# Kernel tuning notes

Hardware: AMD Instinct MI355X
Metric: run time of the kernel (lower is better)

## Reference

```python
import jax, jax.numpy as jnp
import numpy as np

D_MODEL = 1024
NUM_HEADS = 16
DEPTH = D_MODEL // NUM_HEADS  # 64
BATCH = 2
SEQ = 2048


def setup_inputs() -> dict:
    key = jax.random.key(0)
    ks = jax.random.split(key, 11)
    s = 0.02
    return {
        "q": jax.random.normal(ks[0], (BATCH, SEQ, D_MODEL), dtype=jnp.float32),
        "k": jax.random.normal(ks[1], (BATCH, SEQ, D_MODEL), dtype=jnp.float32),
        "v": jax.random.normal(ks[2], (BATCH, SEQ, D_MODEL), dtype=jnp.float32),
        "wq": jax.random.normal(ks[3], (D_MODEL, D_MODEL), dtype=jnp.float32) * s,
        "bq": jnp.zeros((D_MODEL,), dtype=jnp.float32),
        "wk": jax.random.normal(ks[4], (D_MODEL, D_MODEL), dtype=jnp.float32) * s,
        "bk": jnp.zeros((D_MODEL,), dtype=jnp.float32),
        "wv": jax.random.normal(ks[5], (D_MODEL, D_MODEL), dtype=jnp.float32) * s,
        "bv": jnp.zeros((D_MODEL,), dtype=jnp.float32),
        "wo": jax.random.normal(ks[6], (D_MODEL, D_MODEL), dtype=jnp.float32) * s,
        "bo": jnp.zeros((D_MODEL,), dtype=jnp.float32),
    }


def reference(q, k, v, wq, bq, wk, bk, wv, bv, wo, bo):
    B = q.shape[0]
    # QKV projections, then split heads: (B, S, H, D)
    qh = (q @ wq + bq).reshape(B, -1, NUM_HEADS, DEPTH)
    kh = (k @ wk + bk).reshape(B, -1, NUM_HEADS, DEPTH)
    vh = (v @ wv + bv).reshape(B, -1, NUM_HEADS, DEPTH)

    inv_sqrt_dk = 1.0 / jnp.sqrt(jnp.float32(DEPTH))
    # scores: (B, Lq, Lk, H)
    scores = jnp.einsum('blhd,bjhd->bljh', qh, kh) * inv_sqrt_dk
    attn = jax.nn.softmax(scores, axis=2)
    # NOTE: original code divides by sqrt(dk) a SECOND time after softmax (faithful quirk)
    attn = attn * inv_sqrt_dk
    out = jnp.einsum('bljh,bjhe->blhe', attn, vh).reshape(B, -1, NUM_HEADS * DEPTH)
    return out @ wo + bo
```

## Files before the change

### kernel.cpp

```cpp
#include <hip/hip_runtime.h>
#include <math.h>

#define D_MODEL 1024
#define NHEADS 16
#define DH 64
#define BATCH 2
#define SEQ 2048
#define M_TOTAL (BATCH * SEQ)

typedef __attribute__((ext_vector_type(8))) short bf16x8;
typedef __attribute__((ext_vector_type(4))) float f32x4;
typedef __attribute__((ext_vector_type(16))) float f32x16;
typedef __attribute__((ext_vector_type(8))) unsigned short ushort8;
typedef unsigned short u16;
typedef unsigned int u32;

#define SCALE_Q 0.18033688f

static __device__ __forceinline__ u16 f2bf(float x) {
  unsigned int u = __float_as_uint(x);
  unsigned int r = (u + 0x7fffu + ((u >> 16) & 1u)) >> 16;
  return (u16)r;
}
static __device__ __forceinline__ u32 pk2bf(float a, float b) {
  return (u32)f2bf(a) | ((u32)f2bf(b) << 16);
}
static __device__ __forceinline__ u32 pkhu(float a, float b) {
  u32 ua = __float_as_uint(a) + 0x8000u;
  u32 ub = __float_as_uint(b) + 0x8000u;
  return (ua >> 16) | (ub & 0xffff0000u);
}
static __device__ __forceinline__ float exp2fast(float x) {
  return __builtin_amdgcn_exp2f(x);
}

static __device__ __forceinline__ void gl_lds16(const u16* g, u16* l) {
  __builtin_amdgcn_global_load_lds(
      (const __attribute__((address_space(1))) u32*)g,
      (__attribute__((address_space(3))) u32*)l, 16, 0, 0);
}

__global__ __launch_bounds__(256) void cvt_kernel(
    const float* __restrict__ q, const float* __restrict__ k, const float* __restrict__ v,
    u16* __restrict__ qb, u16* __restrict__ kb, u16* __restrict__ vb) {
  const int z = blockIdx.z;
  const float* src = (z == 0) ? q : (z == 1) ? k : v;
  u16* dst = (z == 0) ? qb : (z == 1) ? kb : vb;
  const size_t i = ((size_t)blockIdx.x * 256 + threadIdx.x) * 8;
  float4 a = *reinterpret_cast<const float4*>(src + i);
  float4 b = *reinterpret_cast<const float4*>(src + i + 4);
  u32 o0 = pk2bf(a.x, a.y), o1 = pk2bf(a.z, a.w);
  u32 o2 = pk2bf(b.x, b.y), o3 = pk2bf(b.z, b.w);
  *reinterpret_cast<uint4*>(dst + i) = make_uint4(o0, o1, o2, o3);
}

__global__ __launch_bounds__(256) void wtrans_kernel(
    const float* __restrict__ w0, const float* __restrict__ w1,
    const float* __restrict__ w2, const float* __restrict__ w3,
    u16* __restrict__ t0, u16* __restrict__ t1,
    u16* __restrict__ t2, u16* __restrict__ t3) {
  __shared__ float tf[64 * 68];
  const int z = blockIdx.z;
  const float* w = (z == 0) ? w0 : (z == 1) ? w1 : (z == 2) ? w2 : w3;
  u16* wt = (z == 0) ? t0 : (z == 1) ? t1 : (z == 2) ? t2 : t3;
  const int n0 = blockIdx.x * 64, k0 = blockIdx.y * 64;
  const int tid = threadIdx.x;
  const int kl = tid >> 4, nq = (tid & 15) * 4;
#pragma unroll
  for (int c = 0; c < 4; ++c) {
    float4 v = *reinterpret_cast<const float4*>(
        &w[(size_t)(k0 + kl + c * 16) * 1024 + n0 + nq]);
    *reinterpret_cast<float4*>(&tf[(kl + c * 16) * 68 + nq]) = v;
  }
  __syncthreads();
  const int n = tid & 63, kq = tid >> 6;
  u32 pk[8];
#pragma unroll
  for (int p = 0; p < 8; ++p) {
    float a = tf[(kq * 16 + 2 * p) * 68 + n];
    float b = tf[(kq * 16 + 2 * p + 1) * 68 + n];
    pk[p] = pk2bf(a, b);
  }
  u16* dst = &wt[(size_t)(n0 + n) * 1024 + k0 + kq * 16];
  *reinterpret_cast<uint4*>(dst) = make_uint4(pk[0], pk[1], pk[2], pk[3]);
  *reinterpret_cast<uint4*>(dst + 8) = make_uint4(pk[4], pk[5], pk[6], pk[7]);
}

__global__ __launch_bounds__(256) void qkv_gemm_kernel(
    const u16* __restrict__ qb, const u16* __restrict__ kb, const u16* __restrict__ vb,
    const u16* __restrict__ wqT, const u16* __restrict__ wkT, const u16* __restrict__ wvT,
    const float* __restrict__ bq, const float* __restrict__ bk, const float* __restrict__ bv,
    u16* __restrict__ qh, u16* __restrict__ kh, u16* __restrict__ vhT) {
  __shared__ u16 lds[9216];
  u16* sA = lds;
  u16* sB = lds + 4096;

  const int z = blockIdx.z;
  const u16* A  = (z == 0) ? qb : (z == 1) ? kb : vb;
  const u16* BT = (z == 0) ? wqT : (z == 1) ? wkT : wvT;
  const float* bias = (z == 0) ? bq : (z == 1) ? bk : bv;

  int wg = blockIdx.x + 8 * blockIdx.y;
  wg = (wg & 7) * 32 + (wg >> 3);
  const int m0 = (wg >> 3) * 128;
  const int n0 = (wg & 7) * 128;

  const int tid = threadIdx.x;
  const int w = tid >> 6, l = tid & 63;
  const int wr = w >> 1, wc = w & 1;
  const int n = l & 15, g = l >> 4;

  const u16* Ab = A + (size_t)(m0 + w * 16 + (l >> 2)) * 1024 + (l & 3) * 8;
  const u16* Bb = BT + (size_t)(n0 + w * 16 + (l >> 2)) * 1024 + (l & 3) * 8;
  u16* sAb = sA + w * 512;
  u16* sBb = sB + w * 512;

  f32x4 acc[4][4];
#pragma unroll
  for (int fm = 0; fm < 4; ++fm)
#pragma unroll
    for (int fn = 0; fn < 4; ++fn) acc[fm][fn] = (f32x4)(0.0f);

  for (int kk = 0; kk < 1024; kk += 32) {
    __syncthreads();
    gl_lds16(Ab + kk, sAb);
    gl_lds16(Ab + kk + (size_t)64 * 1024, sAb + 2048);
    gl_lds16(Bb + kk, sBb);
    gl_lds16(Bb + kk + (size_t)64 * 1024, sBb + 2048);
    __syncthreads();
    bf16x8 af[4], bf[4];
#pragma unroll
    for (int f = 0; f < 4; ++f)
      af[f] = *reinterpret_cast<const bf16x8*>(&sA[(wr * 64 + f * 16 + n) * 32 + g * 8]);
#pragma unroll
    for (int f = 0; f < 4; ++f)
      bf[f] = *reinterpret_cast<const bf16x8*>(&sB[(wc * 64 + f * 16 + n) * 32 + g * 8]);
#pragma unroll
    for (int fm = 0; fm < 4; ++fm)
#pragma unroll
      for (int fn = 0; fn < 4; ++fn)
        acc[fm][fn] = __builtin_amdgcn_mfma_f32_16x16x32_bf16(af[fm], bf[fn], acc[fm][fn], 0, 0, 0);
  }

  float bv4[4];
#pragma unroll
  for (int fn = 0; fn < 4; ++fn) bv4[fn] = bias[n0 + wc * 64 + fn * 16 + n];

  if (z < 2) {
    const float scale = (z == 0) ? SCALE_Q : 1.0f;
    u16* dst = (z == 0) ? qh : kh;
#pragma unroll
    for (int fm = 0; fm < 4; ++fm)
#pragma unroll
      for (int fn = 0; fn < 4; ++fn)
#pragma unroll
        for (int rr = 0; rr < 4; ++rr) {
          const int row = m0 + wr * 64 + fm * 16 + g * 4 + rr;
          const int col = n0 + wc * 64 + fn * 16 + n;
          dst[(size_t)row * 1024 + col] = f2bf((acc[fm][fn][rr] + bv4[fn]) * scale);
        }
  } else {
    __syncthreads();
    u16* bw = lds + w * 2304;
    const int hh = (n0 >> 6) + wc;
    const int bb = m0 >> 11;
    const int c = l >> 1, half = l & 1;
    const int sbase = (m0 & 2047) + wr * 64 + half * 32;
#pragma unroll
    for (int p = 0; p < 2; ++p) {
#pragma unroll
      for (int fh = 0; fh < 2; ++fh) {
        const int fn = p * 2 + fh;
#pragma unroll
        for (int fm = 0; fm < 4; ++fm)
#pragma unroll
          for (int rr = 0; rr < 4; ++rr)
            bw[(fh * 16 + n) * 72 + fm * 16 + g * 4 + rr] =
                f2bf(acc[fm][fn][rr] + bv4[fn]);
      }
      __syncthreads();
      u16* gd = vhT + ((size_t)((bb * NHEADS + hh) * DH + p * 32 + c)) * SEQ + sbase;
#pragma unroll
      for (int j = 0; j < 4; ++j)
        *reinterpret_cast<uint4*>(gd + j * 8) =
            *reinterpret_cast<const uint4*>(&bw[c * 72 + half * 32 + j * 8]);
      __syncthreads();
    }
  }
}

__global__ __launch_bounds__(256) void out_gemm_kernel(
    const u16* __restrict__ aob, const u16* __restrict__ woT,
    const float* __restrict__ bo, float* __restrict__ out) {
  __shared__ u16 lds[6144];
  u16* sA = lds;
  u16* sB = lds + 4096;

  int wg = blockIdx.x + 16 * blockIdx.y;
  wg = (wg & 7) * 64 + (wg >> 3);
  const int m0 = (wg >> 4) * 128;
  const int n0 = (wg & 15) * 64;

  const int tid = threadIdx.x;
  const int w = tid >> 6, l = tid & 63;
  const int wr = w >> 1, wc = w & 1;
  const int n = l & 15, g = l >> 4;

  const u16* Ab = aob + (size_t)(m0 + w * 16 + (l >> 2)) * 1024 + (l & 3) * 8;
  const u16* Bb = woT + (size_t)(n0 + w * 16 + (l >> 2)) * 1024 + (l & 3) * 8;
  u16* sAb = sA + w * 512;
  u16* sBb = sB + w * 512;

  f32x4 acc[4][2];
#pragma unroll
  for (int fm = 0; fm < 4; ++fm)
#pragma unroll
    for (int fn = 0; fn < 2; ++fn) acc[fm][fn] = (f32x4)(0.0f);

  for (int kk = 0; kk < 1024; kk += 32) {
    __syncthreads();
    gl_lds16(Ab + kk, sAb);
    gl_lds16(Ab + kk + (size_t)64 * 1024, sAb + 2048);
    gl_lds16(Bb + kk, sBb);
    __syncthreads();
    bf16x8 af[4], bf[2];
#pragma unroll
    for (int f = 0; f < 4; ++f)
      af[f] = *reinterpret_cast<const bf16x8*>(&sA[(wr * 64 + f * 16 + n) * 32 + g * 8]);
#pragma unroll
    for (int f = 0; f < 2; ++f)
      bf[f] = *reinterpret_cast<const bf16x8*>(&sB[(wc * 32 + f * 16 + n) * 32 + g * 8]);
#pragma unroll
    for (int fm = 0; fm < 4; ++fm)
#pragma unroll
      for (int fn = 0; fn < 2; ++fn)
        acc[fm][fn] = __builtin_amdgcn_mfma_f32_16x16x32_bf16(af[fm], bf[fn], acc[fm][fn], 0, 0, 0);
  }

  const float b0 = bo[n0 + wc * 32 + n];
  const float b1 = bo[n0 + wc * 32 + 16 + n];
#pragma unroll
  for (int fm = 0; fm < 4; ++fm)
#pragma unroll
    for (int rr = 0; rr < 4; ++rr) {
      const int row = m0 + wr * 64 + fm * 16 + g * 4 + rr;
      out[(size_t)row * 1024 + n0 + wc * 32 + n] = acc[fm][0][rr] + b0;
      out[(size_t)row * 1024 + n0 + wc * 32 + 16 + n] = acc[fm][1][rr] + b1;
    }
}

#define KT 64
__global__ __launch_bounds__(256, 2) void attn_mfma_kernel(
    const u16* __restrict__ qh, const u16* __restrict__ kh,
    const u16* __restrict__ vhT, u16* __restrict__ aob) {
  const int bid = blockIdx.x;
  const int xcd = bid & 7;
  const int idx = bid >> 3;
  const int bh = (xcd << 2) | (idx >> 4);
  const int qt = idx & 15;
  const int b = bh >> 4, h = bh & 15;

  const int tid = threadIdx.x;
  const int w = tid >> 6, l = tid & 63;
  const int lr = l & 31;
  const int g1 = l >> 5;
  const int q0 = qt * 128 + w * 32;

  __shared__ u16 Ks[2][KT * DH];
  __shared__ u16 Vs[2][DH * KT];
  __shared__ float Ls[4][32];

  bf16x8 qf[4];
#pragma unroll
  for (int kq = 0; kq < 4; ++kq)
    qf[kq] = *reinterpret_cast<const bf16x8*>(
        &qh[((size_t)(b * SEQ + q0 + lr)) * D_MODEL + h * DH + kq * 16 + g1 * 8]);

  f32x16 O0 = (f32x16)(0.0f), O1 = (f32x16)(0.0f);
  float lsum = 0.0f;

  const int srow = tid >> 2, sq = tid & 3;
  const u16* kp0 = kh + (size_t)(b * SEQ + srow) * D_MODEL + h * DH + sq * 16;
  const u16* vp0 = vhT + ((size_t)((b * NHEADS + h) * DH + srow)) * SEQ + sq * 16;
  const int sbase = srow * 64 + sq * 16;
  const int sxor = (srow & 7) << 3;
  const int rxor = (lr & 7) << 3;

  ushort8 kr[2], vr[2];
#pragma unroll
  for (int c = 0; c < 2; ++c) {
    kr[c] = *reinterpret_cast<const ushort8*>(kp0 + c * 8);
    vr[c] = *reinterpret_cast<const ushort8*>(vp0 + c * 8);
  }
#pragma unroll
  for (int c = 0; c < 2; ++c) {
    const int sidx = (sbase + c * 8) ^ sxor;
    *reinterpret_cast<ushort8*>(&Ks[0][sidx]) = kr[c];
    *reinterpret_cast<ushort8*>(&Vs[0][sidx]) = vr[c];
  }
  __syncthreads();

  int cur = 0;
  for (int jt = 0; jt < SEQ / KT; ++jt) {
    if (jt + 1 < SEQ / KT) {
      const int off = (jt + 1) * KT;
#pragma unroll
      for (int c = 0; c < 2; ++c) {
        kr[c] = *reinterpret_cast<const ushort8*>(kp0 + (size_t)off * D_MODEL + c * 8);
        vr[c] = *reinterpret_cast<const ushort8*>(vp0 + off + c * 8);
      }
    }

    __builtin_amdgcn_s_setprio(1);
    f32x16 St0 = (f32x16)(0.0f), St1 = (f32x16)(0.0f);
#pragma unroll
    for (int kq = 0; kq < 4; ++kq) {
      const int coff = kq * 16 + g1 * 8;
      bf16x8 kf0 = *reinterpret_cast<const bf16x8*>(&Ks[cur][(lr * 64 + coff) ^ rxor]);
      bf16x8 kf1 = *reinterpret_cast<const bf16x8*>(&Ks[cur][((32 + lr) * 64 + coff) ^ rxor]);
      St0 = __builtin_amdgcn_mfma_f32_32x32x16_bf16(kf0, qf[kq], St0, 0, 0, 0);
      St1 = __builtin_amdgcn_mfma_f32_32x32x16_bf16(kf1, qf[kq], St1, 0, 0, 0);
    }
    __builtin_amdgcn_s_setprio(0);

    u32 U0[8], U1[8];
#pragma unroll
    for (int s = 0; s < 8; ++s) {
      float a0 = exp2fast(St0[2 * s]), b0 = exp2fast(St0[2 * s + 1]);
      float a1 = exp2fast(St1[2 * s]), b1 = exp2fast(St1[2 * s + 1]);
      lsum += (a0 + b0) + (a1 + b1);
      U0[s] = pkhu(a0, b0);
      U1[s] = pkhu(a1, b1);
    }

    __builtin_amdgcn_s_setprio(1);
#pragma unroll
    for (int kb2 = 0; kb2 < 2; ++kb2) {
#pragma unroll
      for (int m16 = 0; m16 < 2; ++m16) {
        union { u32 u[4]; bf16x8 v; } pa;
        if (kb2 == 0) {
          pa.u[0] = U0[m16 * 4 + 0]; pa.u[1] = U0[m16 * 4 + 1];
          pa.u[2] = U0[m16 * 4 + 2]; pa.u[3] = U0[m16 * 4 + 3];
        } else {
          pa.u[0] = U1[m16 * 4 + 0]; pa.u[1] = U1[m16 * 4 + 1];
          pa.u[2] = U1[m16 * 4 + 2]; pa.u[3] = U1[m16 * 4 + 3];
        }
        const int koff = kb2 * 32 + m16 * 16 + g1 * 4;
        union { u32 u[4]; bf16x8 v; } vb0, vb1;
        *reinterpret_cast<uint2*>(&vb0.u[0]) =
            *reinterpret_cast<const uint2*>(&Vs[cur][(lr * 64 + koff) ^ rxor]);
        *reinterpret_cast<uint2*>(&vb0.u[2]) =
            *reinterpret_cast<const uint2*>(&Vs[cur][(lr * 64 + koff + 8) ^ rxor]);
        *reinterpret_cast<uint2*>(&vb1.u[0]) =
            *reinterpret_cast<const uint2*>(&Vs[cur][((32 + lr) * 64 + koff) ^ rxor]);
        *reinterpret_cast<uint2*>(&vb1.u[2]) =
            *reinterpret_cast<const uint2*>(&Vs[cur][((32 + lr) * 64 + koff + 8) ^ rxor]);
        O0 = __builtin_amdgcn_mfma_f32_32x32x16_bf16(pa.v, vb0.v, O0, 0, 0, 0);
        O1 = __builtin_amdgcn_mfma_f32_32x32x16_bf16(pa.v, vb1.v, O1, 0, 0, 0);
      }
    }
    __builtin_amdgcn_s_setprio(0);

    if (jt + 1 < SEQ / KT) {
#pragma unroll
      for (int c = 0; c < 2; ++c) {
        const int sidx = (sbase + c * 8) ^ sxor;
        *reinterpret_cast<ushort8*>(&Ks[cur ^ 1][sidx]) = kr[c];
        *reinterpret_cast<ushort8*>(&Vs[cur ^ 1][sidx]) = vr[c];
      }
    }
    __syncthreads();
    cur ^= 1;
  }

  lsum += (float)__shfl_xor(lsum, 32);
  if (g1 == 0) Ls[w][lr] = lsum;
  float invr[16];
#pragma unroll
  for (int c = 0; c < 4; ++c) {
    float4 lv = *reinterpret_cast<const float4*>(&Ls[w][c * 8 + g1 * 4]);
    invr[c * 4 + 0] = 0.125f / lv.x;
    invr[c * 4 + 1] = 0.125f / lv.y;
    invr[c * 4 + 2] = 0.125f / lv.z;
    invr[c * 4 + 3] = 0.125f / lv.w;
  }
#pragma unroll
  for (int dblk = 0; dblk < 2; ++dblk) {
#pragma unroll
    for (int s = 0; s < 8; ++s) {
      const int r0 = 2 * s, r1 = 2 * s + 1;
      float x0 = (dblk ? O1[r0] : O0[r0]) * invr[r0];
      float x1 = (dblk ? O1[r1] : O0[r1]) * invr[r1];
      const int row0 = q0 + (r0 & 3) + 8 * (r0 >> 2) + 4 * g1;
      const int row1 = q0 + (r1 & 3) + 8 * (r1 >> 2) + 4 * g1;
      const int col = h * DH + dblk * 32 + lr;
      aob[((size_t)(b * SEQ + row0)) * D_MODEL + col] = f2bf(x0);
      aob[((size_t)(b * SEQ + row1)) * D_MODEL + col] = f2bf(x1);
    }
  }
}

extern "C" void kernel_launch(void* const* d_in, const int* in_sizes, int n_in,
                              void* d_out, int out_size, void* d_ws, size_t ws_size,
                              hipStream_t stream) {
  const float* q  = (const float*)d_in[0];
  const float* k  = (const float*)d_in[1];
  const float* v  = (const float*)d_in[2];
  const float* wq = (const float*)d_in[3];
  const float* bq = (const float*)d_in[4];
  const float* wk = (const float*)d_in[5];
  const float* bk = (const float*)d_in[6];
  const float* wv = (const float*)d_in[7];
  const float* bv = (const float*)d_in[8];
  const float* wo = (const float*)d_in[9];
  const float* bo = (const float*)d_in[10];
  float* out = (float*)d_out;

  const size_t wcount = (size_t)D_MODEL * D_MODEL;
  const size_t tcount = (size_t)M_TOTAL * D_MODEL;
  u16* wqT = (u16*)d_ws;
  u16* wkT = wqT + wcount;
  u16* wvT = wkT + wcount;
  u16* woT = wvT + wcount;
  u16* qb  = woT + wcount;
  u16* kb  = qb + tcount;
  u16* vb  = kb + tcount;
  u16* qh  = vb + tcount;
  u16* kh  = qh + tcount;
  u16* vhT = kh + tcount;
  u16* aob = qb;

  dim3 blk(256);

  cvt_kernel<<<dim3(2048, 1, 3), blk, 0, stream>>>(q, k, v, qb, kb, vb);
  wtrans_kernel<<<dim3(16, 16, 4), blk, 0, stream>>>(wq, wk, wv, wo, wqT, wkT, wvT, woT);

  qkv_gemm_kernel<<<dim3(8, 32, 3), blk, 0, stream>>>(
      qb, kb, vb, wqT, wkT, wvT, bq, bk, bv, qh, kh, vhT);

  attn_mfma_kernel<<<dim3(512), dim3(256), 0, stream>>>(qh, kh, vhT, aob);

  out_gemm_kernel<<<dim3(16, 32), blk, 0, stream>>>(aob, woT, bo, out);
}
```

Measured before the change: 136.7 us.

## Merge prep kernels, compute softmax row sums via MFMA, use perm packing

Fuses the fp32-to-bf16 activation conversion and weight transpose into one launch, saving a kernel launch and its tail. In attention, the softmax denominator is now accumulated by an extra MFMA of the bf16 probabilities against a ones vector. This replaces the per-element VALU adds, the cross-lane shuffle and the LDS exchange. The bf16 packing uses a single v_perm. The trade-off is one extra MFMA per PV step and row sums built from rounded bf16 probabilities. The prep grid also launches many idle blocks for the weight slices.

```diff
diff --git a/kernel.cpp b/kernel.cpp
--- a/kernel.cpp
+++ b/kernel.cpp
@@ -26,9 +26,8 @@
   return (u32)f2bf(a) | ((u32)f2bf(b) << 16);
 }
 static __device__ __forceinline__ u32 pkhu(float a, float b) {
-  u32 ua = __float_as_uint(a) + 0x8000u;
-  u32 ub = __float_as_uint(b) + 0x8000u;
-  return (ua >> 16) | (ub & 0xffff0000u);
+  return __builtin_amdgcn_perm(__float_as_uint(b) + 0x8000u,
+                               __float_as_uint(a) + 0x8000u, 0x07060302u);
 }
 static __device__ __forceinline__ float exp2fast(float x) {
   return __builtin_amdgcn_exp2f(x);
@@ -40,37 +39,38 @@
       (__attribute__((address_space(3))) u32*)l, 16, 0, 0);
 }
 
-__global__ __launch_bounds__(256) void cvt_kernel(
+__global__ __launch_bounds__(256) void prep_kernel(
     const float* __restrict__ q, const float* __restrict__ k, const float* __restrict__ v,
-    u16* __restrict__ qb, u16* __restrict__ kb, u16* __restrict__ vb) {
-  const int z = blockIdx.z;
-  const float* src = (z == 0) ? q : (z == 1) ? k : v;
-  u16* dst = (z == 0) ? qb : (z == 1) ? kb : vb;
-  const size_t i = ((size_t)blockIdx.x * 256 + threadIdx.x) * 8;
-  float4 a = *reinterpret_cast<const float4*>(src + i);
-  float4 b = *reinterpret_cast<const float4*>(src + i + 4);
-  u32 o0 = pk2bf(a.x, a.y), o1 = pk2bf(a.z, a.w);
-  u32 o2 = pk2bf(b.x, b.y), o3 = pk2bf(b.z, b.w);
-  *reinterpret_cast<uint4*>(dst + i) = make_uint4(o0, o1, o2, o3);
-}
-
-__global__ __launch_bounds__(256) void wtrans_kernel(
+    u16* __restrict__ qb, u16* __restrict__ kb, u16* __restrict__ vb,
     const float* __restrict__ w0, const float* __restrict__ w1,
     const float* __restrict__ w2, const float* __restrict__ w3,
     u16* __restrict__ t0, u16* __restrict__ t1,
     u16* __restrict__ t2, u16* __restrict__ t3) {
   __shared__ float tf[64 * 68];
   const int z = blockIdx.z;
-  const float* w = (z == 0) ? w0 : (z == 1) ? w1 : (z == 2) ? w2 : w3;
-  u16* wt = (z == 0) ? t0 : (z == 1) ? t1 : (z == 2) ? t2 : t3;
-  const int n0 = blockIdx.x * 64, k0 = blockIdx.y * 64;
   const int tid = threadIdx.x;
+  if (z < 3) {
+    const float* src = (z == 0) ? q : (z == 1) ? k : v;
+    u16* dst = (z == 0) ? qb : (z == 1) ? kb : vb;
+    const size_t i = ((size_t)blockIdx.x * 256 + tid) * 8;
+    float4 a = *reinterpret_cast<const float4*>(src + i);
+    float4 b = *reinterpret_cast<const float4*>(src + i + 4);
+    u32 o0 = pk2bf(a.x, a.y), o1 = pk2bf(a.z, a.w);
+    u32 o2 = pk2bf(b.x, b.y), o3 = pk2bf(b.z, b.w);
+    *reinterpret_cast<uint4*>(dst + i) = make_uint4(o0, o1, o2, o3);
+    return;
+  }
+  if (blockIdx.x >= 256) return;
+  const int zz = z - 3;
+  const float* w = (zz == 0) ? w0 : (zz == 1) ? w1 : (zz == 2) ? w2 : w3;
+  u16* wt = (zz == 0) ? t0 : (zz == 1) ? t1 : (zz == 2) ? t2 : t3;
+  const int n0 = (blockIdx.x & 15) * 64, k0 = (blockIdx.x >> 4) * 64;
   const int kl = tid >> 4, nq = (tid & 15) * 4;
 #pragma unroll
   for (int c = 0; c < 4; ++c) {
-    float4 v = *reinterpret_cast<const float4*>(
+    float4 vv = *reinterpret_cast<const float4*>(
         &w[(size_t)(k0 + kl + c * 16) * 1024 + n0 + nq]);
-    *reinterpret_cast<float4*>(&tf[(kl + c * 16) * 68 + nq]) = v;
+    *reinterpret_cast<float4*>(&tf[(kl + c * 16) * 68 + nq]) = vv;
   }
   __syncthreads();
   const int n = tid & 63, kq = tid >> 6;
@@ -268,7 +268,9 @@
 
   __shared__ u16 Ks[2][KT * DH];
   __shared__ u16 Vs[2][DH * KT];
-  __shared__ float Ls[4][32];
+
+  union { u32 u[4]; bf16x8 v; } onesu;
+  onesu.u[0] = onesu.u[1] = onesu.u[2] = onesu.u[3] = 0x3F803F80u;
 
   bf16x8 qf[4];
 #pragma unroll
@@ -276,8 +278,7 @@
     qf[kq] = *reinterpret_cast<const bf16x8*>(
         &qh[((size_t)(b * SEQ + q0 + lr)) * D_MODEL + h * DH + kq * 16 + g1 * 8]);
 
-  f32x16 O0 = (f32x16)(0.0f), O1 = (f32x16)(0.0f);
-  float lsum = 0.0f;
+  f32x16 O0 = (f32x16)(0.0f), O1 = (f32x16)(0.0f), L0 = (f32x16)(0.0f);
 
   const int srow = tid >> 2, sq = tid & 3;
   const u16* kp0 = kh + (size_t)(b * SEQ + srow) * D_MODEL + h * DH + sq * 16;
@@ -328,7 +329,6 @@
     for (int s = 0; s < 8; ++s) {
       float a0 = exp2fast(St0[2 * s]), b0 = exp2fast(St0[2 * s + 1]);
       float a1 = exp2fast(St1[2 * s]), b1 = exp2fast(St1[2 * s + 1]);
-      lsum += (a0 + b0) + (a1 + b1);
       U0[s] = pkhu(a0, b0);
       U1[s] = pkhu(a1, b1);
     }
@@ -358,6 +358,7 @@
             *reinterpret_cast<const uint2*>(&Vs[cur][((32 + lr) * 64 + koff + 8) ^ rxor]);
         O0 = __builtin_amdgcn_mfma_f32_32x32x16_bf16(pa.v, vb0.v, O0, 0, 0, 0);
         O1 = __builtin_amdgcn_mfma_f32_32x32x16_bf16(pa.v, vb1.v, O1, 0, 0, 0);
+        L0 = __builtin_amdgcn_mfma_f32_32x32x16_bf16(pa.v, onesu.v, L0, 0, 0, 0);
       }
     }
     __builtin_amdgcn_s_setprio(0);
@@ -374,17 +375,9 @@
     cur ^= 1;
   }
 
-  lsum += (float)__shfl_xor(lsum, 32);
-  if (g1 == 0) Ls[w][lr] = lsum;
   float invr[16];
 #pragma unroll
-  for (int c = 0; c < 4; ++c) {
-    float4 lv = *reinterpret_cast<const float4*>(&Ls[w][c * 8 + g1 * 4]);
-    invr[c * 4 + 0] = 0.125f / lv.x;
-    invr[c * 4 + 1] = 0.125f / lv.y;
-    invr[c * 4 + 2] = 0.125f / lv.z;
-    invr[c * 4 + 3] = 0.125f / lv.w;
-  }
+  for (int r = 0; r < 16; ++r) invr[r] = 0.125f / L0[r];
 #pragma unroll
   for (int dblk = 0; dblk < 2; ++dblk) {
 #pragma unroll
@@ -433,13 +426,13 @@
 
   dim3 blk(256);
 
-  cvt_kernel<<<dim3(2048, 1, 3), blk, 0, stream>>>(q, k, v, qb, kb, vb);
-  wtrans_kernel<<<dim3(16, 16, 4), blk, 0, stream>>>(wq, wk, wv, wo, wqT, wkT, wvT, woT);
+  prep_kernel<<<dim3(2048, 1, 7), blk, 0, stream>>>(
+      q, k, v, qb, kb, vb, wq, wk, wv, wo, wqT, wkT, wvT, woT);
 
   qkv_gemm_kernel<<<dim3(8, 32, 3), blk, 0, stream>>>(
       qb, kb, vb, wqT, wkT, wvT, bq, bk, bv, qh, kh, vhT);
 
-  attn_mfma_kernel<<<dim3(512), dim3(256), 0, stream>>>(qh, kh, vhT, aob);
+  attn_mfma_kernel<<<dim3(512), blk, 0, stream>>>(qh, kh, vhT, aob);
 
   out_gemm_kernel<<<dim3(16, 32), blk, 0, stream>>>(aob, woT, bo, out);
 }
```

Result: faster. 133.5 us (-2.3%).
